# Optimization experiments

Hardware: AMD Instinct MI355X
Metric: run time of the kernel (lower is better)

Reference implementation:

```python
import jax, jax.numpy as jnp
import numpy as np

B, T, C, A, D, H, W = 2, 16, 64, 64, 32, 32, 32  # batch, timepoints, channels, att_features, spatial


def setup_inputs() -> dict:
    key = jax.random.key(0)
    ks = jax.random.split(key, 7)
    s = 1.0 / np.sqrt(C)
    return {
        "x": jax.random.normal(ks[0], (B, T, C, D, H, W), dtype=jnp.float32),
        "Wk": jax.random.normal(ks[1], (A, C), dtype=jnp.float32) * s,
        "bk": jax.random.normal(ks[2], (A,), dtype=jnp.float32) * s,
        "Wq": jax.random.normal(ks[3], (A, C), dtype=jnp.float32) * s,
        "bq": jax.random.normal(ks[4], (A,), dtype=jnp.float32) * s,
        "Wv": jax.random.normal(ks[5], (C, C), dtype=jnp.float32) * s,
        "bv": jax.random.normal(ks[6], (C,), dtype=jnp.float32) * s,
    }


def reference(x, Wk, bk, Wq, bq, Wv, bv):
    # kernel=1 Conv3d == pointwise channel mixing. Project and move spatial
    # dims to the front exactly like movedim((3,4,5),(1,2,3)):
    # result layout [B, D, H, W, T, out_ch].
    def proj(Wt, bt):
        return jnp.einsum('btcdhw,oc->bdhwto', x, Wt) + bt

    k = proj(Wk, bk)  # [B,D,H,W,T,A]
    q = proj(Wq, bq)  # [B,D,H,W,T,A]
    v = proj(Wv, bv)  # [B,D,H,W,T,C]

    scale = 1.0 / np.sqrt(float(Wk.shape[0]))  # sqrt(att_features)
    att = jnp.einsum('bdhwta,bdhwsa->bdhwts', k, q) * scale  # [B,D,H,W,T,T]
    # norm = partial(softmax, dim=1) on the 6-D tensor -> softmax over spatial D axis
    att_map = jax.nn.softmax(att, axis=1)

    # features = (value^T @ att_map)^T: feat[...,s,c] = sum_t v[...,t,c] * att_map[...,t,s]
    feat = jnp.einsum('bdhwtc,bdhwts->bdhwsc', v, att_map)  # [B,D,H,W,T,C]
    # movedim((1,2,3),(3,4,5)): back to [B, T, C, D, H, W]
    return jnp.transpose(feat, (0, 4, 5, 1, 2, 3))
```

## Files before the change

### kernel.cpp

```cpp
#include <hip/hip_runtime.h>
#include <hip/hip_fp16.h>

typedef short v8s __attribute__((ext_vector_type(8)));
typedef float v4f __attribute__((ext_vector_type(4)));
typedef float v2f __attribute__((ext_vector_type(2)));

#define NSP 32768
#define XSTR 2056
#define WS_ZP_B  65536ull
#define WS_ATT_B 16777216ull

__device__ __forceinline__ unsigned short f2bf(float f) {
  union { float f; unsigned u; } v; v.f = f;
  unsigned r = v.u + 0x7fffu + ((v.u >> 16) & 1u);
  return (unsigned short)(r >> 16);
}
__device__ __forceinline__ unsigned pk(float a, float b) {
  return (unsigned)f2bf(a) | ((unsigned)f2bf(b) << 16);
}
__device__ __forceinline__ unsigned pkh(float a, float b) {
  union { __half2 h; unsigned u; } c; c.h = __floats2half2_rn(a, b); return c.u;
}
__device__ __forceinline__ float2 uph(unsigned u) {
  union { unsigned u; __half2 h; } c; c.u = u; return __half22float2(c.h);
}

union UF8 { v8s v; unsigned u[4]; uint4 q; };


__global__ __launch_bounds__(512) void prep_kernel(
    const float* __restrict__ Wk, const float* __restrict__ bk,
    const float* __restrict__ Wq, const float* __restrict__ bq,
    const float* __restrict__ Wv, unsigned* __restrict__ ws) {
  __shared__ float sWk[4096], sWq[4096], sWv[4096], sbk[64], sbq[64];
  for (int i = threadIdx.x; i < 4096; i += 512) { sWk[i] = Wk[i]; sWq[i] = Wq[i]; sWv[i] = Wv[i]; }
  if (threadIdx.x < 64) { sbk[threadIdx.x] = bk[threadIdx.x]; sbq[threadIdx.x] = bq[threadIdx.x]; }
  __syncthreads();
  for (int task = threadIdx.x; task < 18 * 64; task += 512) {
    int f = task >> 6, lane = task & 63;
    int i16 = lane & 15, g = lane >> 4;
    unsigned short e[8];
    #pragma unroll
    for (int j = 0; j < 8; ++j) {
      int k = (((j >> 2) << 4) + 4 * g + (j & 3));
      float acc = 0.f;
      if (f < 8) {
        int row = ((f >> 1) << 4) + i16;
        int cc  = ((f & 1) << 5) + k;
        for (int a = 0; a < 64; ++a) acc += sWk[a * 64 + row] * sWq[a * 64 + cc];
      } else if (f < 10) {
        int c = ((f - 8) << 5) + k;
        if (i16 == 0)      { for (int a = 0; a < 64; ++a) acc += sWk[a * 64 + c] * sbq[a]; }
        else if (i16 == 1) { for (int a = 0; a < 64; ++a) acc += sbk[a] * sWq[a * 64 + c]; }
      } else {
        int c  = (((f - 10) >> 1) << 4) + i16;
        int cp = (((f - 10) & 1) << 5) + k;
        acc = sWv[c * 64 + cp];
      }
      e[j] = f2bf(acc);
    }
    unsigned* dst = ws + (size_t)(f * 64 + lane) * 4;
    dst[0] = e[0] | ((unsigned)e[1] << 16);
    dst[1] = e[2] | ((unsigned)e[3] << 16);
    dst[2] = e[4] | ((unsigned)e[5] << 16);
    dst[3] = e[6] | ((unsigned)e[7] << 16);
  }
  if (threadIdx.x == 0) {
    float beta = 0.f;
    for (int a = 0; a < 64; ++a) beta += sbk[a] * sbq[a];
    ((float*)ws)[18 * 256] = beta;
  }
}

#define S2L 0.18033688011112042f

#define DECODE256() \
  int bid = (int)blockIdx.x; \
  int b = bid & 1, dc = (bid >> 1) & 3, h = bid >> 3; \
  const int d0 = dc << 3; \
  const size_t base0 = (size_t)b * 33554432 + h * 32;

#define DECODE512() \
  int bid = (int)blockIdx.x; \
  int b = bid & 1, dcc = (bid >> 1) & 7, h = bid >> 4; \
  const int d0 = dcc << 2; \
  const size_t base0 = (size_t)b * 33554432 + h * 32;

#define STAGE_DEFS() \
  const int w2 = tid & 15; \
  const int rp0 = tid >> 4; \
  v2f sA[8], sB[8]; \
  auto issueH = [&](int d, int half) { \
    const float* xp = x + base0 + (size_t)d * 1024; \
    _Pragma("unroll") \
    for (int i = 0; i < 8; ++i) { \
      int rp = half * 256 + (i << 5) + rp0; \
      const float* r0 = xp + (size_t)(2 * rp) * NSP + 2 * w2; \
      sA[i] = *(const v2f*)r0; \
      sB[i] = *(const v2f*)(r0 + NSP); \
    } \
  }; \
  auto writeH = [&](unsigned char* BUF, int half) { \
    _Pragma("unroll") \
    for (int i = 0; i < 8; ++i) { \
      int rp = half * 256 + (i << 5) + rp0; \
      int t = rp >> 5, c = (rp & 31) << 1; \
      int off = (t << 7) + (((c << 1)) ^ ((t & 7) << 4)); \
      *(unsigned*)(&BUF[(2 * w2) * XSTR + off])     = pk(sA[i].x, sB[i].x); \
      *(unsigned*)(&BUF[(2 * w2 + 1) * XSTR + off]) = pk(sA[i].y, sB[i].y); \
    } \
  };

#define LOADX_DEF() \
  auto loadX = [&](const unsigned char* BUF, int loc, v8s fX[2]) { \
    const unsigned char* bp = &BUF[loc * XSTR + (i16 << 7)]; \
    const int sw = (i16 & 7) << 4; \
    _Pragma("unroll") \
    for (int kc = 0; kc < 2; ++kc) { \
      union { v8s v; unsigned long long dd[2]; } u; \
      int o = (kc << 6) + (g << 3); \
      u.dd[0] = *(const unsigned long long*)(bp + (o ^ sw)); \
      u.dd[1] = *(const unsigned long long*)(bp + ((o + 32) ^ sw)); \
      fX[kc] = u.v; \
    } \
  };

#define LDF_DEF() \
  auto ldf = [&](int f) -> v8s { \
    union { v8s v; uint4 q; } u; \
    u.q = *(const uint4*)&Wm[(f << 8) + (lane << 2)]; \
    return u.v; \
  };

#define ATTOF_DEF() \
  auto attOf = [&](const v8s fX[2]) -> v4f { \
    v4f accW[4]; \
    _Pragma("unroll") \
    for (int tr = 0; tr < 4; ++tr) { \
      v8s m0 = ldf(2 * tr), m1 = ldf(2 * tr + 1); \
      v4f a = {0.f, 0.f, 0.f, 0.f}; \
      a = __builtin_amdgcn_mfma_f32_16x16x32_bf16(m0, fX[0], a, 0, 0, 0); \
      a = __builtin_amdgcn_mfma_f32_16x16x32_bf16(m1, fX[1], a, 0, 0, 0); \
      accW[tr] = a; \
    } \
    v8s u0 = ldf(8), u1 = ldf(9); \
    v4f au = {0.f, 0.f, 0.f, 0.f}; \
    au = __builtin_amdgcn_mfma_f32_16x16x32_bf16(u0, fX[0], au, 0, 0, 0); \
    au = __builtin_amdgcn_mfma_f32_16x16x32_bf16(u1, fX[1], au, 0, 0, 0); \
    float a1v = au[0] + beta; \
    float a2v = au[1]; \
    float a2s = __shfl(a2v, i16); \
    v4f att; \
    _Pragma("unroll") \
    for (int j = 0; j < 4; ++j) att[j] = __shfl(a1v, 4 * g + j) + a2s; \
    _Pragma("unroll") \
    for (int kc = 0; kc < 2; ++kc) { \
      UF8 w; \
      w.u[0] = pk(accW[2 * kc][0], accW[2 * kc][1]); \
      w.u[1] = pk(accW[2 * kc][2], accW[2 * kc][3]); \
      w.u[2] = pk(accW[2 * kc + 1][0], accW[2 * kc + 1][1]); \
      w.u[3] = pk(accW[2 * kc + 1][2], accW[2 * kc + 1][3]); \
      att = __builtin_amdgcn_mfma_f32_16x16x32_bf16(fX[kc], w.v, att, 0, 0, 0); \
    } \
    return att; \
  };

#define FEATQ(tn, FB) do { \
  _Pragma("unroll") \
  for (int l = 0; l < 4; ++l) { \
    int wq = 4 * wv + l; \
    UF8 fP; fP.u[0] = Pp[l][0]; fP.u[1] = Pp[l][1]; fP.u[2] = 0; fP.u[3] = 0; \
    UF8 fV; fV.u[0] = vp[l][2 * (tn)]; fV.u[1] = vp[l][2 * (tn) + 1]; fV.u[2] = 0; fV.u[3] = 0; \
    v4f ft = {0.f, 0.f, 0.f, 0.f}; \
    ft = __builtin_amdgcn_mfma_f32_16x16x32_bf16(fP.v, fV.v, ft, 0, 0, 0); \
    _Pragma("unroll") \
    for (int j = 0; j < 4; ++j) { \
      int r = (4 * g + j) * 16 + i16; \
      (FB)[r * 33 + (wq ^ g)] = ft[j]; \
    } \
  } \
} while (0)

__global__ __launch_bounds__(512) void pass1_z(
    const float* __restrict__ x, const unsigned* __restrict__ ws,
    float* __restrict__ zp, unsigned* __restrict__ attw) {
  __shared__ __align__(16) unsigned char Xd[2][65792];
  __shared__ unsigned Wm[2560];

  const int tid = (int)threadIdx.x;
  const int lane = tid & 63, wv = tid >> 6;
  const int i16 = lane & 15, g = lane >> 4;
  DECODE256();

  for (int o = tid; o < 2560; o += 512) Wm[o] = ws[o];
  const float beta = ((const float*)ws)[4608];

  STAGE_DEFS();
  LOADX_DEF();
  LDF_DEF();
  ATTOF_DEF();

  auto doLoc = [&](const unsigned char* cur, int d, int l, float Zl[4]) {
    v8s fX[2]; loadX(cur, 4 * wv + l, fX);
    v4f att = attOf(fX);
    float s0 = att[0] * S2L, s1 = att[1] * S2L;
    float s2 = att[2] * S2L, s3 = att[3] * S2L;
    Zl[0] += exp2f(s0); Zl[1] += exp2f(s1);
    Zl[2] += exp2f(s2); Zl[3] += exp2f(s3);
    uint2 av; av.x = pkh(s0, s1); av.y = pkh(s2, s3);
    const size_t ls = ((size_t)((b << 5) + h) * 32 + d) * 32 + (4 * wv + l);
    *(uint2*)(attw + ls * 128 + lane * 2) = av;
  };

  float Z[4][4] = {};
  issueH(d0, 0); writeH(Xd[0], 0);
  issueH(d0, 1); writeH(Xd[0], 1);
  __syncthreads();
  for (int ii = 0; ii < 8; ++ii) {
    const int d = d0 + ii;
    unsigned char* cur = Xd[ii & 1];
    unsigned char* nxt = Xd[(ii & 1) ^ 1];
    if (ii < 7) issueH(d + 1, 0);
    doLoc(cur, d, 0, Z[0]);
    doLoc(cur, d, 1, Z[1]);
    if (ii < 7) { writeH(nxt, 0); issueH(d + 1, 1); }
    doLoc(cur, d, 2, Z[2]);
    doLoc(cur, d, 3, Z[3]);
    if (ii < 7) writeH(nxt, 1);
    __syncthreads();
  }
  const int locg = b * 1024 + h * 32 + 4 * wv;
  #pragma unroll
  for (int l = 0; l < 4; ++l)
    #pragma unroll
    for (int j = 0; j < 4; ++j)
      zp[(((size_t)dc * 2048 + locg + l) << 8) + (4 * g + j) * 16 + i16] = Z[l][j];
}

__global__ __launch_bounds__(512) void pass2_out(
    const float* __restrict__ x, const float* __restrict__ bv,
    const unsigned* __restrict__ ws, const float* __restrict__ zp,
    const unsigned* __restrict__ attw, float* __restrict__ out) {
  __shared__ __align__(16) unsigned char Xd[2][67584];
  __shared__ unsigned Wm[2048];

  const int tid = (int)threadIdx.x;
  const int lane = tid & 63, wv = tid >> 6;
  const int i16 = lane & 15, g = lane >> 4;
  DECODE512();

  for (int o = tid; o < 2048; o += 512) Wm[o] = ws[2560 + o];
  float bvv[4];
  #pragma unroll
  for (int tn = 0; tn < 4; ++tn) bvv[tn] = bv[i16 + 16 * tn];

  float iZ[4][4];
  #pragma unroll
  for (int l = 0; l < 4; ++l) {
    const int locg = b * 1024 + h * 32 + 4 * wv + l;
    #pragma unroll
    for (int j = 0; j < 4; ++j) {
      float s = 0.f;
      #pragma unroll
      for (int c2 = 0; c2 < 4; ++c2)
        s += zp[(((size_t)c2 * 2048 + locg) << 8) + (4 * g + j) * 16 + i16];
      iZ[l][j] = 1.f / s;
    }
  }

  STAGE_DEFS();
  LOADX_DEF();

  auto lfv = [&](int f) -> v8s {
    union { v8s v; uint4 q; } u;
    u.q = *(const uint4*)&Wm[(f << 8) + (lane << 2)];
    return u.v;
  };
  auto loadAtt = [&](int d, uint2* dst) {
    #pragma unroll
    for (int l = 0; l < 4; ++l) {
      const size_t ls = ((size_t)((b << 5) + h) * 32 + d) * 32 + (4 * wv + l);
      dst[l] = *(const uint2*)(attw + ls * 128 + lane * 2);
    }
  };

  auto storeQ = [&](int tn, int d, const float* FB) {
    float* op = out + base0 + (size_t)d * 1024 + (size_t)(16 * tn) * NSP;
    const int w4 = tid & 7, rr = tid >> 3;
    #pragma unroll
    for (int it = 0; it < 4; ++it) {
      int r = (it << 6) + rr;
      const float* fp = &FB[r * 33 + (w4 << 2)];
      float4 val;
      val.x = fp[0 ^ it]; val.y = fp[1 ^ it]; val.z = fp[2 ^ it]; val.w = fp[3 ^ it];
      *(float4*)(op + (size_t)((r >> 4) * 64 + (r & 15)) * NSP + (w4 << 2)) = val;
    }
  };

  uint2 ar[4];
  loadAtt(d0, ar);
  issueH(d0, 0); writeH(Xd[0], 0);
  issueH(d0, 1); writeH(Xd[0], 1);
  for (int ii = 0; ii < 4; ++ii) {
    const int d = d0 + ii;
    unsigned char* A = Xd[ii & 1];
    unsigned char* B = Xd[(ii & 1) ^ 1];
    __syncthreads();

    unsigned Pp[4][2], vp[4][8];
    if (ii < 3) issueH(d + 1, 0);
    #pragma unroll
    for (int l = 0; l < 4; ++l) {
      if (l == 2 && ii < 3) { writeH(B, 0); issueH(d + 1, 1); }
      float2 f01 = uph(ar[l].x), f23 = uph(ar[l].y);
      float p0 = exp2f(f01.x) * iZ[l][0], p1 = exp2f(f01.y) * iZ[l][1];
      float p2 = exp2f(f23.x) * iZ[l][2], p3 = exp2f(f23.y) * iZ[l][3];
      Pp[l][0] = pk(p0, p1); Pp[l][1] = pk(p2, p3);
      v8s fX[2]; loadX(A, 4 * wv + l, fX);
      #pragma unroll
      for (int tn = 0; tn < 4; ++tn) {
        v8s wa = lfv(2 * tn), wb = lfv(2 * tn + 1);
        v4f a = {bvv[tn], bvv[tn], bvv[tn], bvv[tn]};
        a = __builtin_amdgcn_mfma_f32_16x16x32_bf16(fX[0], wa, a, 0, 0, 0);
        a = __builtin_amdgcn_mfma_f32_16x16x32_bf16(fX[1], wb, a, 0, 0, 0);
        vp[l][2 * tn] = pk(a[0], a[1]); vp[l][2 * tn + 1] = pk(a[2], a[3]);
      }
    }
    if (ii < 3) writeH(B, 1);
    __syncthreads();

    float* FbA = (float*)A;
    float* FbB = FbA + 8448;
    uint2 arN[4];
    FEATQ(0, FbA);
    __syncthreads();
    storeQ(0, d, FbA);
    if (ii < 3) loadAtt(d + 1, arN);
    FEATQ(1, FbB);
    __syncthreads();
    storeQ(1, d, FbB); FEATQ(2, FbA);
    __syncthreads();
    storeQ(2, d, FbA); FEATQ(3, FbB);
    __syncthreads();
    storeQ(3, d, FbB);
    if (ii < 3) { ar[0] = arN[0]; ar[1] = arN[1]; ar[2] = arN[2]; ar[3] = arN[3]; }
  }
}

extern "C" void kernel_launch(void* const* d_in, const int* in_sizes, int n_in,
                              void* d_out, int out_size, void* d_ws, size_t ws_size,
                              hipStream_t stream) {
  const float* x  = (const float*)d_in[0];
  const float* Wk = (const float*)d_in[1];
  const float* bk = (const float*)d_in[2];
  const float* Wq = (const float*)d_in[3];
  const float* bq = (const float*)d_in[4];
  const float* Wv = (const float*)d_in[5];
  const float* bv = (const float*)d_in[6];
  float* out = (float*)d_out;
  unsigned* ws = (unsigned*)d_ws;
  float*    zp   = (float*)((char*)d_ws + WS_ZP_B);
  unsigned* attw = (unsigned*)((char*)d_ws + WS_ATT_B);

  prep_kernel<<<1, 512, 0, stream>>>(Wk, bk, Wq, bq, Wv, ws);
  pass1_z<<<256, 512, 0, stream>>>(x, ws, zp, attw);
  pass2_out<<<512, 512, 0, stream>>>(x, bv, ws, zp, attw, out);
}
```

Baseline: 274.1 us.

## Split pass2 blocks over half-width W tiles to double grid and cut LDS

The output pass now gives each block half of the W row (16 locations instead of 32), so the grid doubles from 512 to 1024 blocks. Per-block LDS staging shrinks by about half and per-thread register arrays shrink too. The aim is higher occupancy, likely two blocks per CU, and better latency hiding. Staging, the feature scatter and the store path were reworked with a new XOR swizzle to keep LDS conflict-free at 16-wide rows. The cost is shorter 64-byte contiguous global segments per row and duplicated weight and bias loading per block.

```diff
diff --git a/kernel.cpp b/kernel.cpp
--- a/kernel.cpp
+++ b/kernel.cpp
@@ -80,11 +80,14 @@
   const int d0 = dc << 3; \
   const size_t base0 = (size_t)b * 33554432 + h * 32;
 
-#define DECODE512() \
+#define DECODE1024() \
   int bid = (int)blockIdx.x; \
-  int b = bid & 1, dcc = (bid >> 1) & 7, h = bid >> 4; \
+  int b   = bid & 1; \
+  int whp = (bid >> 3) & 1; \
+  int dcc = ((bid >> 1) & 3) | (((bid >> 4) & 1) << 2); \
+  int h   = bid >> 5; \
   const int d0 = dcc << 2; \
-  const size_t base0 = (size_t)b * 33554432 + h * 32;
+  const size_t base0 = (size_t)b * 33554432 + h * 32 + whp * 16;
 
 #define STAGE_DEFS() \
   const int w2 = tid & 15; \
@@ -104,6 +107,31 @@
     _Pragma("unroll") \
     for (int i = 0; i < 8; ++i) { \
       int rp = half * 256 + (i << 5) + rp0; \
+      int t = rp >> 5, c = (rp & 31) << 1; \
+      int off = (t << 7) + (((c << 1)) ^ ((t & 7) << 4)); \
+      *(unsigned*)(&BUF[(2 * w2) * XSTR + off])     = pk(sA[i].x, sB[i].x); \
+      *(unsigned*)(&BUF[(2 * w2 + 1) * XSTR + off]) = pk(sA[i].y, sB[i].y); \
+    } \
+  };
+
+#define STAGE16_DEFS() \
+  const int w2 = tid & 7; \
+  const int rp0 = tid >> 3; \
+  v2f sA[4], sB[4]; \
+  auto issueH = [&](int d, int half) { \
+    const float* xp = x + base0 + (size_t)d * 1024; \
+    _Pragma("unroll") \
+    for (int i = 0; i < 4; ++i) { \
+      int rp = half * 256 + (i << 6) + rp0; \
+      const float* r0 = xp + (size_t)(2 * rp) * NSP + 2 * w2; \
+      sA[i] = *(const v2f*)r0; \
+      sB[i] = *(const v2f*)(r0 + NSP); \
+    } \
+  }; \
+  auto writeH = [&](unsigned char* BUF, int half) { \
+    _Pragma("unroll") \
+    for (int i = 0; i < 4; ++i) { \
+      int rp = half * 256 + (i << 6) + rp0; \
       int t = rp >> 5, c = (rp & 31) << 1; \
       int off = (t << 7) + (((c << 1)) ^ ((t & 7) << 4)); \
       *(unsigned*)(&BUF[(2 * w2) * XSTR + off])     = pk(sA[i].x, sB[i].x); \
@@ -165,10 +193,10 @@
     return att; \
   };
 
-#define FEATQ(tn, FB) do { \
+#define FEATQ16(tn, FB) do { \
   _Pragma("unroll") \
-  for (int l = 0; l < 4; ++l) { \
-    int wq = 4 * wv + l; \
+  for (int l = 0; l < 2; ++l) { \
+    int wq = 2 * wv + l; \
     UF8 fP; fP.u[0] = Pp[l][0]; fP.u[1] = Pp[l][1]; fP.u[2] = 0; fP.u[3] = 0; \
     UF8 fV; fV.u[0] = vp[l][2 * (tn)]; fV.u[1] = vp[l][2 * (tn) + 1]; fV.u[2] = 0; fV.u[3] = 0; \
     v4f ft = {0.f, 0.f, 0.f, 0.f}; \
@@ -176,7 +204,7 @@
     _Pragma("unroll") \
     for (int j = 0; j < 4; ++j) { \
       int r = (4 * g + j) * 16 + i16; \
-      (FB)[r * 33 + (wq ^ g)] = ft[j]; \
+      (FB)[r * 16 + (wq ^ (((g + (i16 >> 1)) & 3) << 2))] = ft[j]; \
     } \
   } \
 } while (0)
@@ -241,23 +269,23 @@
     const float* __restrict__ x, const float* __restrict__ bv,
     const unsigned* __restrict__ ws, const float* __restrict__ zp,
     const unsigned* __restrict__ attw, float* __restrict__ out) {
-  __shared__ __align__(16) unsigned char Xd[2][67584];
+  __shared__ __align__(16) unsigned char Xd[2][32896];
   __shared__ unsigned Wm[2048];
 
   const int tid = (int)threadIdx.x;
   const int lane = tid & 63, wv = tid >> 6;
   const int i16 = lane & 15, g = lane >> 4;
-  DECODE512();
+  DECODE1024();
 
   for (int o = tid; o < 2048; o += 512) Wm[o] = ws[2560 + o];
   float bvv[4];
   #pragma unroll
   for (int tn = 0; tn < 4; ++tn) bvv[tn] = bv[i16 + 16 * tn];
 
-  float iZ[4][4];
+  float iZ[2][4];
   #pragma unroll
-  for (int l = 0; l < 4; ++l) {
-    const int locg = b * 1024 + h * 32 + 4 * wv + l;
+  for (int l = 0; l < 2; ++l) {
+    const int locg = b * 1024 + h * 32 + whp * 16 + 2 * wv + l;
     #pragma unroll
     for (int j = 0; j < 4; ++j) {
       float s = 0.f;
@@ -268,7 +296,7 @@
     }
   }
 
-  STAGE_DEFS();
+  STAGE16_DEFS();
   LOADX_DEF();
 
   auto lfv = [&](int f) -> v8s {
@@ -278,26 +306,25 @@
   };
   auto loadAtt = [&](int d, uint2* dst) {
     #pragma unroll
-    for (int l = 0; l < 4; ++l) {
-      const size_t ls = ((size_t)((b << 5) + h) * 32 + d) * 32 + (4 * wv + l);
+    for (int l = 0; l < 2; ++l) {
+      const size_t ls = ((size_t)((b << 5) + h) * 32 + d) * 32 + whp * 16 + 2 * wv + l;
       dst[l] = *(const uint2*)(attw + ls * 128 + lane * 2);
     }
   };
 
   auto storeQ = [&](int tn, int d, const float* FB) {
     float* op = out + base0 + (size_t)d * 1024 + (size_t)(16 * tn) * NSP;
-    const int w4 = tid & 7, rr = tid >> 3;
-    #pragma unroll
-    for (int it = 0; it < 4; ++it) {
-      int r = (it << 6) + rr;
-      const float* fp = &FB[r * 33 + (w4 << 2)];
-      float4 val;
-      val.x = fp[0 ^ it]; val.y = fp[1 ^ it]; val.z = fp[2 ^ it]; val.w = fp[3 ^ it];
-      *(float4*)(op + (size_t)((r >> 4) * 64 + (r & 15)) * NSP + (w4 << 2)) = val;
-    }
-  };
-
-  uint2 ar[4];
+    const int w4 = tid & 3, rr = tid >> 2;
+    #pragma unroll
+    for (int it = 0; it < 2; ++it) {
+      int r = (it << 7) + rr;
+      int q = ((r >> 6) + ((r & 15) >> 1)) & 3;
+      float4 val = *(const float4*)&FB[r * 16 + 4 * w4];
+      *(float4*)(op + (size_t)(((r >> 4) << 6) + (r & 15)) * NSP + 4 * (w4 ^ q)) = val;
+    }
+  };
+
+  uint2 ar[2];
   loadAtt(d0, ar);
   issueH(d0, 0); writeH(Xd[0], 0);
   issueH(d0, 1); writeH(Xd[0], 1);
@@ -307,16 +334,16 @@
     unsigned char* B = Xd[(ii & 1) ^ 1];
     __syncthreads();
 
-    unsigned Pp[4][2], vp[4][8];
+    unsigned Pp[2][2], vp[2][8];
     if (ii < 3) issueH(d + 1, 0);
     #pragma unroll
-    for (int l = 0; l < 4; ++l) {
-      if (l == 2 && ii < 3) { writeH(B, 0); issueH(d + 1, 1); }
+    for (int l = 0; l < 2; ++l) {
+      if (l == 1 && ii < 3) { writeH(B, 0); issueH(d + 1, 1); }
       float2 f01 = uph(ar[l].x), f23 = uph(ar[l].y);
       float p0 = exp2f(f01.x) * iZ[l][0], p1 = exp2f(f01.y) * iZ[l][1];
       float p2 = exp2f(f23.x) * iZ[l][2], p3 = exp2f(f23.y) * iZ[l][3];
       Pp[l][0] = pk(p0, p1); Pp[l][1] = pk(p2, p3);
-      v8s fX[2]; loadX(A, 4 * wv + l, fX);
+      v8s fX[2]; loadX(A, 2 * wv + l, fX);
       #pragma unroll
       for (int tn = 0; tn < 4; ++tn) {
         v8s wa = lfv(2 * tn), wb = lfv(2 * tn + 1);
@@ -330,20 +357,20 @@
     __syncthreads();
 
     float* FbA = (float*)A;
-    float* FbB = FbA + 8448;
-    uint2 arN[4];
-    FEATQ(0, FbA);
+    float* FbB = FbA + 4096;
+    uint2 arN[2];
+    FEATQ16(0, FbA);
     __syncthreads();
     storeQ(0, d, FbA);
     if (ii < 3) loadAtt(d + 1, arN);
-    FEATQ(1, FbB);
-    __syncthreads();
-    storeQ(1, d, FbB); FEATQ(2, FbA);
-    __syncthreads();
-    storeQ(2, d, FbA); FEATQ(3, FbB);
+    FEATQ16(1, FbB);
+    __syncthreads();
+    storeQ(1, d, FbB); FEATQ16(2, FbA);
+    __syncthreads();
+    storeQ(2, d, FbA); FEATQ16(3, FbB);
     __syncthreads();
     storeQ(3, d, FbB);
-    if (ii < 3) { ar[0] = arN[0]; ar[1] = arN[1]; ar[2] = arN[2]; ar[3] = arN[3]; }
+    if (ii < 3) { ar[0] = arN[0]; ar[1] = arN[1]; }
   }
 }
 
@@ -364,5 +391,5 @@
 
   prep_kernel<<<1, 512, 0, stream>>>(Wk, bk, Wq, bq, Wv, ws);
   pass1_z<<<256, 512, 0, stream>>>(x, ws, zp, attw);
-  pass2_out<<<512, 512, 0, stream>>>(x, bv, ws, zp, attw, out);
-}
+  pass2_out<<<1024, 512, 0, stream>>>(x, bv, ws, zp, attw, out);
+}
```

Result: slower. 339.5 us (+23.9%).

## Compute V projection in pass1 and store bf16 V for pass2

Applied to the files above, without the earlier changes.

Moves the value projection out of the second pass into the first pass, which already stages x, and writes V as packed bf16 to workspace. Pass2 then reads compact V instead of re-reading fp32 x and recomputing, so it needs less shared memory and no staging or V MFMAs. In exchange pass1 does more MFMA work and an extra global write, and pass2 now depends on a workspace round trip.

```diff
diff --git a/kernel.cpp b/kernel.cpp
--- a/kernel.cpp
+++ b/kernel.cpp
@@ -9,6 +9,7 @@
 #define XSTR 2056
 #define WS_ZP_B  65536ull
 #define WS_ATT_B 16777216ull
+#define WS_V_B   50331648ull
 
 __device__ __forceinline__ unsigned short f2bf(float f) {
   union { float f; unsigned u; } v; v.f = f;
@@ -182,18 +183,22 @@
 } while (0)
 
 __global__ __launch_bounds__(512) void pass1_z(
-    const float* __restrict__ x, const unsigned* __restrict__ ws,
-    float* __restrict__ zp, unsigned* __restrict__ attw) {
+    const float* __restrict__ x, const float* __restrict__ bv,
+    const unsigned* __restrict__ ws, float* __restrict__ zp,
+    unsigned* __restrict__ attw, unsigned* __restrict__ vw) {
   __shared__ __align__(16) unsigned char Xd[2][65792];
-  __shared__ unsigned Wm[2560];
+  __shared__ unsigned Wm[4608];
 
   const int tid = (int)threadIdx.x;
   const int lane = tid & 63, wv = tid >> 6;
   const int i16 = lane & 15, g = lane >> 4;
   DECODE256();
 
-  for (int o = tid; o < 2560; o += 512) Wm[o] = ws[o];
+  for (int o = tid; o < 4608; o += 512) Wm[o] = ws[o];
   const float beta = ((const float*)ws)[4608];
+  float bvv[4];
+  #pragma unroll
+  for (int tn = 0; tn < 4; ++tn) bvv[tn] = bv[i16 + 16 * tn];
 
   STAGE_DEFS();
   LOADX_DEF();
@@ -207,9 +212,31 @@
     float s2 = att[2] * S2L, s3 = att[3] * S2L;
     Zl[0] += exp2f(s0); Zl[1] += exp2f(s1);
     Zl[2] += exp2f(s2); Zl[3] += exp2f(s3);
+    const size_t ls = ((size_t)((b << 5) + h) * 32 + d) * 32 + (4 * wv + l);
     uint2 av; av.x = pkh(s0, s1); av.y = pkh(s2, s3);
-    const size_t ls = ((size_t)((b << 5) + h) * 32 + d) * 32 + (4 * wv + l);
     *(uint2*)(attw + ls * 128 + lane * 2) = av;
+    uint4 o0, o1;
+    {
+      v4f a;
+      a = (v4f){bvv[0], bvv[0], bvv[0], bvv[0]};
+      a = __builtin_amdgcn_mfma_f32_16x16x32_bf16(fX[0], ldf(10), a, 0, 0, 0);
+      a = __builtin_amdgcn_mfma_f32_16x16x32_bf16(fX[1], ldf(11), a, 0, 0, 0);
+      o0.x = pk(a[0], a[1]); o0.y = pk(a[2], a[3]);
+      a = (v4f){bvv[1], bvv[1], bvv[1], bvv[1]};
+      a = __builtin_amdgcn_mfma_f32_16x16x32_bf16(fX[0], ldf(12), a, 0, 0, 0);
+      a = __builtin_amdgcn_mfma_f32_16x16x32_bf16(fX[1], ldf(13), a, 0, 0, 0);
+      o0.z = pk(a[0], a[1]); o0.w = pk(a[2], a[3]);
+      a = (v4f){bvv[2], bvv[2], bvv[2], bvv[2]};
+      a = __builtin_amdgcn_mfma_f32_16x16x32_bf16(fX[0], ldf(14), a, 0, 0, 0);
+      a = __builtin_amdgcn_mfma_f32_16x16x32_bf16(fX[1], ldf(15), a, 0, 0, 0);
+      o1.x = pk(a[0], a[1]); o1.y = pk(a[2], a[3]);
+      a = (v4f){bvv[3], bvv[3], bvv[3], bvv[3]};
+      a = __builtin_amdgcn_mfma_f32_16x16x32_bf16(fX[0], ldf(16), a, 0, 0, 0);
+      a = __builtin_amdgcn_mfma_f32_16x16x32_bf16(fX[1], ldf(17), a, 0, 0, 0);
+      o1.z = pk(a[0], a[1]); o1.w = pk(a[2], a[3]);
+    }
+    uint4* vpd = (uint4*)vw + ls * 128 + lane * 2;
+    vpd[0] = o0; vpd[1] = o1;
   };
 
   float Z[4][4] = {};
@@ -238,21 +265,14 @@
 }
 
 __global__ __launch_bounds__(512) void pass2_out(
-    const float* __restrict__ x, const float* __restrict__ bv,
-    const unsigned* __restrict__ ws, const float* __restrict__ zp,
-    const unsigned* __restrict__ attw, float* __restrict__ out) {
-  __shared__ __align__(16) unsigned char Xd[2][67584];
-  __shared__ unsigned Wm[2048];
+    const float* __restrict__ zp, const unsigned* __restrict__ attw,
+    const unsigned* __restrict__ vw, float* __restrict__ out) {
+  __shared__ float Fb2[2][8448];
 
   const int tid = (int)threadIdx.x;
   const int lane = tid & 63, wv = tid >> 6;
   const int i16 = lane & 15, g = lane >> 4;
   DECODE512();
-
-  for (int o = tid; o < 2048; o += 512) Wm[o] = ws[2560 + o];
-  float bvv[4];
-  #pragma unroll
-  for (int tn = 0; tn < 4; ++tn) bvv[tn] = bv[i16 + 16 * tn];
 
   float iZ[4][4];
   #pragma unroll
@@ -268,19 +288,19 @@
     }
   }
 
-  STAGE_DEFS();
-  LOADX_DEF();
-
-  auto lfv = [&](int f) -> v8s {
-    union { v8s v; uint4 q; } u;
-    u.q = *(const uint4*)&Wm[(f << 8) + (lane << 2)];
-    return u.v;
+  auto lsOf = [&](int d, int l) -> size_t {
+    return ((size_t)((b << 5) + h) * 32 + d) * 32 + (4 * wv + l);
   };
   auto loadAtt = [&](int d, uint2* dst) {
     #pragma unroll
+    for (int l = 0; l < 4; ++l)
+      dst[l] = *(const uint2*)(attw + lsOf(d, l) * 128 + lane * 2);
+  };
+  auto loadV = [&](int d, uint4* a4, uint4* b4) {
+    #pragma unroll
     for (int l = 0; l < 4; ++l) {
-      const size_t ls = ((size_t)((b << 5) + h) * 32 + d) * 32 + (4 * wv + l);
-      dst[l] = *(const uint2*)(attw + ls * 128 + lane * 2);
+      const uint4* vpd = (const uint4*)vw + lsOf(d, l) * 128 + lane * 2;
+      a4[l] = vpd[0]; b4[l] = vpd[1];
     }
   };
 
@@ -297,53 +317,37 @@
     }
   };
 
-  uint2 ar[4];
+  uint2 ar[4]; uint4 vA[4], vB[4];
   loadAtt(d0, ar);
-  issueH(d0, 0); writeH(Xd[0], 0);
-  issueH(d0, 1); writeH(Xd[0], 1);
+  loadV(d0, vA, vB);
   for (int ii = 0; ii < 4; ++ii) {
     const int d = d0 + ii;
-    unsigned char* A = Xd[ii & 1];
-    unsigned char* B = Xd[(ii & 1) ^ 1];
-    __syncthreads();
-
     unsigned Pp[4][2], vp[4][8];
-    if (ii < 3) issueH(d + 1, 0);
     #pragma unroll
     for (int l = 0; l < 4; ++l) {
-      if (l == 2 && ii < 3) { writeH(B, 0); issueH(d + 1, 1); }
       float2 f01 = uph(ar[l].x), f23 = uph(ar[l].y);
       float p0 = exp2f(f01.x) * iZ[l][0], p1 = exp2f(f01.y) * iZ[l][1];
       float p2 = exp2f(f23.x) * iZ[l][2], p3 = exp2f(f23.y) * iZ[l][3];
       Pp[l][0] = pk(p0, p1); Pp[l][1] = pk(p2, p3);
-      v8s fX[2]; loadX(A, 4 * wv + l, fX);
+      vp[l][0] = vA[l].x; vp[l][1] = vA[l].y; vp[l][2] = vA[l].z; vp[l][3] = vA[l].w;
+      vp[l][4] = vB[l].x; vp[l][5] = vB[l].y; vp[l][6] = vB[l].z; vp[l][7] = vB[l].w;
+    }
+    uint2 arN[4]; uint4 vAn[4], vBn[4];
+    FEATQ(0, Fb2[0]);
+    __syncthreads();
+    storeQ(0, d, Fb2[0]);
+    if (ii < 3) { loadAtt(d + 1, arN); loadV(d + 1, vAn, vBn); }
+    FEATQ(1, Fb2[1]);
+    __syncthreads();
+    storeQ(1, d, Fb2[1]); FEATQ(2, Fb2[0]);
+    __syncthreads();
+    storeQ(2, d, Fb2[0]); FEATQ(3, Fb2[1]);
+    __syncthreads();
+    storeQ(3, d, Fb2[1]);
+    if (ii < 3) {
       #pragma unroll
-      for (int tn = 0; tn < 4; ++tn) {
-        v8s wa = lfv(2 * tn), wb = lfv(2 * tn + 1);
-        v4f a = {bvv[tn], bvv[tn], bvv[tn], bvv[tn]};
-        a = __builtin_amdgcn_mfma_f32_16x16x32_bf16(fX[0], wa, a, 0, 0, 0);
-        a = __builtin_amdgcn_mfma_f32_16x16x32_bf16(fX[1], wb, a, 0, 0, 0);
-        vp[l][2 * tn] = pk(a[0], a[1]); vp[l][2 * tn + 1] = pk(a[2], a[3]);
-      }
-    }
-    if (ii < 3) writeH(B, 1);
-    __syncthreads();
-
-    float* FbA = (float*)A;
-    float* FbB = FbA + 8448;
-    uint2 arN[4];
-    FEATQ(0, FbA);
-    __syncthreads();
-    storeQ(0, d, FbA);
-    if (ii < 3) loadAtt(d + 1, arN);
-    FEATQ(1, FbB);
-    __syncthreads();
-    storeQ(1, d, FbB); FEATQ(2, FbA);
-    __syncthreads();
-    storeQ(2, d, FbA); FEATQ(3, FbB);
-    __syncthreads();
-    storeQ(3, d, FbB);
-    if (ii < 3) { ar[0] = arN[0]; ar[1] = arN[1]; ar[2] = arN[2]; ar[3] = arN[3]; }
+      for (int l = 0; l < 4; ++l) { ar[l] = arN[l]; vA[l] = vAn[l]; vB[l] = vBn[l]; }
+    }
   }
 }
 
@@ -361,8 +365,9 @@
   unsigned* ws = (unsigned*)d_ws;
   float*    zp   = (float*)((char*)d_ws + WS_ZP_B);
   unsigned* attw = (unsigned*)((char*)d_ws + WS_ATT_B);
+  unsigned* vw   = (unsigned*)((char*)d_ws + WS_V_B);
 
   prep_kernel<<<1, 512, 0, stream>>>(Wk, bk, Wq, bq, Wv, ws);
-  pass1_z<<<256, 512, 0, stream>>>(x, ws, zp, attw);
-  pass2_out<<<512, 512, 0, stream>>>(x, bv, ws, zp, attw, out);
-}
+  pass1_z<<<256, 512, 0, stream>>>(x, bv, ws, zp, attw, vw);
+  pass2_out<<<512, 512, 0, stream>>>(zp, attw, vw, out);
+}
```

Result: no change. 273.7 us (-0.2%).
